# Kernel optimization log

Hardware: AMD Instinct MI355X
Metric: run time of the kernel (lower is better)

The kernel has to match this reference:

```python
import jax, jax.numpy as jnp
import numpy as np

TEMP = 0.01            # entropy temperature
THRESH = 0.92          # hamming similarity threshold
BETA = 0.25            # commitment weight
ENT_W = 0.1            # entropy loss weight


def _l2_normalize(x, axis=-1, eps=1e-12):
    n = jnp.sqrt(jnp.sum(x * x, axis=axis, keepdims=True))
    return x / jnp.maximum(n, eps)


def _entropy_loss(affinity):
    # affinity: [N, K] codebook affinities (cosine similarities)
    fa = affinity / TEMP
    probs = jax.nn.softmax(fa, axis=-1)
    log_probs = jax.nn.log_softmax(fa + 1e-5, axis=-1)
    avg_probs = jnp.mean(probs, axis=0)
    avg_entropy = -jnp.sum(avg_probs * jnp.log(avg_probs + 1e-5))
    sample_entropy = -jnp.mean(jnp.sum(probs * log_probs, axis=-1))
    return sample_entropy - avg_entropy


def _hamming_consistency_loss(input_blocks, z_e):
    # binary occupancy: non-air voxels -> 1
    binary = (jnp.argmax(input_blocks, axis=1) != 0).astype(jnp.float32)  # [B,24,24,24]
    B = binary.shape[0]
    # faithful to torch: plain reshapes (no transpose)
    patterns = binary.reshape(B, 6, 4, 6, 4, 6, 4).reshape(B, 6, 6, 6, 64).reshape(-1, 64)
    N = patterns.shape[0]
    P = patterns
    # pairwise hamming distance via two Gram matmuls
    ham = P @ (1.0 - P).T + (1.0 - P) @ P.T          # [N,N]
    sim = 1.0 - ham / 64.0
    mask = (sim > THRESH) & (~jnp.eye(N, dtype=bool))
    W = jax.lax.stop_gradient(jnp.where(mask, sim, 0.0))  # detached weights
    # pre-quant embeddings per chunk, l2-normalized; cosine distance matrix
    emb = jnp.transpose(z_e, (0, 2, 3, 4, 1)).reshape(N, -1)  # [N, C]
    en = _l2_normalize(emb, axis=1)
    cos = en @ en.T                                   # [N,N]
    dist = 1.0 - cos
    return jnp.sum(dist * W) / (jnp.sum(W) + 1e-8)


def setup_inputs() -> dict:
    key = jax.random.key(0)
    k1, k2, k3 = jax.random.split(key, 3)
    input_blocks = jax.random.normal(k1, (16, 32, 24, 24, 24), dtype=jnp.float32)
    z_e = jax.random.normal(k2, (16, 256, 6, 6, 6), dtype=jnp.float32)
    codebook = jax.random.normal(k3, (1024, 256), dtype=jnp.float32)
    return {"input_blocks": input_blocks, "z_e": z_e, "codebook": codebook}


def reference(input_blocks, z_e, codebook):
    B, C, H, W, D = z_e.shape
    z = jnp.transpose(z_e, (0, 2, 3, 4, 1)).reshape(-1, C)   # [N, C]
    zn = _l2_normalize(z, axis=1)
    en = _l2_normalize(codebook, axis=1)                      # [K, C]
    affinity = zn @ en.T                                      # [N, K]
    idx = jnp.argmax(affinity, axis=1)                        # max cosine == min L2 on sphere
    z_q = en[idx]                                             # [N, C]
    sg = jax.lax.stop_gradient
    codebook_loss = jnp.mean((z_q - sg(zn)) ** 2)
    commit_loss = BETA * jnp.mean((sg(z_q) - zn) ** 2)
    ent_loss = ENT_W * _entropy_loss(affinity)
    ham_loss = _hamming_consistency_loss(input_blocks, z_e)
    loss = codebook_loss + commit_loss + ent_loss + ham_loss
    # straight-through estimator
    z_q_ste = zn + sg(z_q - zn)
    z_q_out = jnp.transpose(z_q_ste.reshape(B, H, W, D, C), (0, 4, 1, 2, 3))
    return z_q_out, loss, idx
```

## Files before the change

### kernel.cpp

```cpp
#include <hip/hip_runtime.h>
#include <cstdint>
#include <cstddef>

#define N_ROWS 3456
#define C_DIM 256
#define K_CB 1024
#define B_SZ 16
#define SPATIAL 216
#define VOX 13824
#define NCH 32
#define N_GBLK 108
#define N_FBLK 486

typedef __attribute__((ext_vector_type(16))) float f32x16;
typedef __attribute__((ext_vector_type(8))) short bf16x8;

__device__ __forceinline__ unsigned short f2bf_rne(float f) {
    unsigned int u = __float_as_uint(f);
    u += 0x7FFFu + ((u >> 16) & 1u);
    return (unsigned short)(u >> 16);
}
__device__ __forceinline__ float bf2f(unsigned short h) {
    unsigned int u = ((unsigned int)h) << 16;
    return __uint_as_float(u);
}

__device__ __forceinline__ size_t swz(int n, int c) {
    return (size_t)(n >> 5) * 8192 + (size_t)((c >> 3) * 256) + (size_t)((n & 31) * 8) + (c & 7);
}

__global__ __launch_bounds__(256) void k_pre(
        const float* __restrict__ in, const float* __restrict__ cb,
        const float* __restrict__ ze,
        unsigned long long* __restrict__ pats,
        float* __restrict__ scal,
        float* __restrict__ en,
        unsigned short* __restrict__ ehi, unsigned short* __restrict__ elo,
        unsigned short* __restrict__ zhi, unsigned short* __restrict__ zlo) {
    int bid = blockIdx.x;
    int t = threadIdx.x;
    if (bid < 432) {
        if (bid == 0 && t < 16) scal[t] = 0.0f;
        __shared__ unsigned long long wpk[8];
        if (t < 8) wpk[t] = 0ULL;
        __syncthreads();
        int v0i = bid * 512 + t * 2;
        int b = v0i / VOX;
        int r = v0i % VOX;
        const float* p = in + (size_t)b * NCH * VOX + r;
        float2 vals[NCH];
#pragma unroll
        for (int c = 0; c < NCH; ++c)
            vals[c] = *(const float2*)&p[(size_t)c * VOX];
        float m0 = vals[1].x, m1 = vals[1].y;
#pragma unroll
        for (int c = 2; c < NCH; ++c) {
            m0 = fmaxf(m0, vals[c].x);
            m1 = fmaxf(m1, vals[c].y);
        }
        unsigned long long bits = (m0 > vals[0].x ? 1ULL : 0ULL)
                                | (m1 > vals[0].y ? 2ULL : 0ULL);
        atomicOr(&wpk[t >> 5], bits << ((t & 31) * 2));
        __syncthreads();
        if (t < 8) pats[(bid * 512 >> 6) + t] = wpk[t];
        return;
    }
    __shared__ float ws[16];
    if (bid < 1456) {
        int k = bid - 432, c = t;
        float v = cb[k * C_DIM + c];
        float ss = v * v;
#pragma unroll
        for (int off = 32; off > 0; off >>= 1) ss += __shfl_down(ss, off, 64);
        if ((c & 63) == 0) ws[c >> 6] = ss;
        __syncthreads();
        float nrm = fmaxf(sqrtf(ws[0] + ws[1] + ws[2] + ws[3]), 1e-12f);
        float o = v / nrm;
        en[k * C_DIM + c] = o;
        unsigned short h = f2bf_rne(o);
        size_t off = swz(k, c);
        ehi[off] = h;
        elo[off] = f2bf_rne(o - bf2f(h));
    } else {
        int zb = bid - 1456;
        int n0 = zb * 4;
        int b = n0 / SPATIAL, s0 = n0 - b * SPATIAL;
        int c = t, w = t >> 6, lane = t & 63;
        float4 v4 = *(const float4*)&ze[((size_t)(b * C_DIM + c)) * SPATIAL + s0];
        float q0 = v4.x * v4.x, q1 = v4.y * v4.y, q2 = v4.z * v4.z, q3 = v4.w * v4.w;
#pragma unroll
        for (int off = 32; off > 0; off >>= 1) {
            q0 += __shfl_down(q0, off, 64);
            q1 += __shfl_down(q1, off, 64);
            q2 += __shfl_down(q2, off, 64);
            q3 += __shfl_down(q3, off, 64);
        }
        if (lane == 0) {
            ws[w * 4 + 0] = q0; ws[w * 4 + 1] = q1;
            ws[w * 4 + 2] = q2; ws[w * 4 + 3] = q3;
        }
        __syncthreads();
        float vv[4] = {v4.x, v4.y, v4.z, v4.w};
#pragma unroll
        for (int j = 0; j < 4; ++j) {
            float nrm = fmaxf(sqrtf(ws[j] + ws[4 + j] + ws[8 + j] + ws[12 + j]), 1e-12f);
            float o = vv[j] / nrm;
            unsigned short h = f2bf_rne(o);
            size_t off = swz(n0 + j, c);
            zhi[off] = h;
            zlo[off] = f2bf_rne(o - bf2f(h));
        }
    }
}

__global__ __launch_bounds__(512) void k_fat(
        const unsigned short* __restrict__ zhi, const unsigned short* __restrict__ zlo,
        const unsigned short* __restrict__ ehi, const unsigned short* __restrict__ elo,
        const unsigned long long* __restrict__ pats,
        const float* __restrict__ en,
        float* __restrict__ avgp_part, float* __restrict__ scal,
        float* __restrict__ out) {
    __shared__ float zq[32 * 257];
    __shared__ float sm[32][8];
    __shared__ int   si[32][8];
    __shared__ float sS[32][8];
    __shared__ float sT[32][8];
    __shared__ float gm[32];
    __shared__ int   gmi[32];
    __shared__ float invS[32];
    __shared__ float ws8[8];
    __shared__ float hw8[8], hd8[8];
    __shared__ int lastflag;
    unsigned int* done = (unsigned int*)&scal[8];

    int t = threadIdx.x;
    int w = t >> 6, lane = t & 63;
    int half = lane >> 5, l31 = lane & 31;

    int bid0 = blockIdx.x;
    int xcd = bid0 & 7, slot = bid0 >> 3;
    int bid;
    if (bid0 < 432) {
        if (xcd < 2) bid = slot * 2 + xcd;
        else         bid = N_GBLK + slot * 6 + (xcd - 2);
    } else {
        bid = N_GBLK + 324 + (bid0 - 432);
    }

    const bf16x8* __restrict__ Zh = (const bf16x8*)zhi;
    const bf16x8* __restrict__ Zl = (const bf16x8*)zlo;
    const bf16x8* __restrict__ Eh = (const bf16x8*)ehi;
    const bf16x8* __restrict__ El = (const bf16x8*)elo;

    if (bid < N_GBLK) {
        int sa = bid;
        int n0 = bid * 32;
        int boff = (bid * 5) & 15;

        f32x16 acc[4];
#pragma unroll
        for (int q = 0; q < 4; ++q)
#pragma unroll
            for (int e = 0; e < 16; ++e) acc[q][e] = 0.0f;

#pragma unroll
        for (int s = 0; s < 16; ++s) {
            int s16 = (s + boff) & 15;
            int u = s16 * 64 + lane;
            bf16x8 ah = Zh[(size_t)sa * 1024 + u];
            bf16x8 al = Zl[(size_t)sa * 1024 + u];
            bf16x8 bh[4], bl[4];
#pragma unroll
            for (int q = 0; q < 4; ++q) {
                bh[q] = Eh[(size_t)(w * 4 + q) * 1024 + u];
                bl[q] = El[(size_t)(w * 4 + q) * 1024 + u];
            }
#pragma unroll
            for (int q = 0; q < 4; ++q) {
                acc[q] = __builtin_amdgcn_mfma_f32_32x32x16_bf16(ah, bh[q], acc[q], 0, 0, 0);
                acc[q] = __builtin_amdgcn_mfma_f32_32x32x16_bf16(ah, bl[q], acc[q], 0, 0, 0);
                acc[q] = __builtin_amdgcn_mfma_f32_32x32x16_bf16(al, bh[q], acc[q], 0, 0, 0);
            }
        }

#pragma unroll
        for (int g = 0; g < 16; ++g) {
            float m = acc[0][g];
            int mi = w * 128 + l31;
#pragma unroll
            for (int q = 1; q < 4; ++q) {
                float x = acc[q][g];
                int c = w * 128 + q * 32 + l31;
                if (x > m) { m = x; mi = c; }
            }
#pragma unroll
            for (int mask = 1; mask < 32; mask <<= 1) {
                float vo = __shfl_xor(m, mask, 64);
                int   io = __shfl_xor(mi, mask, 64);
                if (vo > m || (vo == m && io < mi)) { m = vo; mi = io; }
            }
            int row = (g & 3) + 8 * (g >> 2) + 4 * half;
            if (l31 == 0) { sm[row][w] = m; si[row][w] = mi; }
        }
        __syncthreads();

        float cmv = 0.0f;
        if (t < 32) {
            float m = sm[t][0];
            int mi = si[t][0];
#pragma unroll
            for (int ww = 1; ww < 8; ++ww) {
                float mw = sm[t][ww];
                int miw = si[t][ww];
                if (mw > m || (mw == m && miw < mi)) { m = mw; mi = miw; }
            }
            gm[t] = m; gmi[t] = mi;
            out[884737 + n0 + t] = (float)mi;
            cmv = 2.0f - 2.0f * m;
        }
        if (w == 0) {
#pragma unroll
            for (int off = 32; off > 0; off >>= 1) cmv += __shfl_down(cmv, off, 64);
            if (lane == 0) atomicAdd(&scal[1], cmv);
        }
        __syncthreads();

#pragma unroll
        for (int g = 0; g < 16; ++g) {
            int row = (g & 3) + 8 * (g >> 2) + 4 * half;
            float gmr = gm[row];
            float S = 0.0f, T = 0.0f;
#pragma unroll
            for (int q = 0; q < 4; ++q) {
                float d = 100.0f * (acc[q][g] - gmr);
                float ee = __expf(d);
                S += ee; T += ee * d;
                acc[q][g] = ee;
            }
#pragma unroll
            for (int mask = 1; mask < 32; mask <<= 1) {
                S += __shfl_xor(S, mask, 64);
                T += __shfl_xor(T, mask, 64);
            }
            if (l31 == 0) { sS[row][w] = S; sT[row][w] = T; }
        }
#pragma unroll
        for (int rr = 0; rr < 4; ++rr) {
            int row = w * 4 + rr;
            int mi = gmi[row];
            float4 g4 = *(const float4*)&en[(size_t)mi * C_DIM + lane * 4];
            zq[row * 257 + lane * 4 + 0] = g4.x;
            zq[row * 257 + lane * 4 + 1] = g4.y;
            zq[row * 257 + lane * 4 + 2] = g4.z;
            zq[row * 257 + lane * 4 + 3] = g4.w;
        }
        __syncthreads();

        float sev = 0.0f;
        if (t < 32) {
            float S = 0.0f, T = 0.0f;
#pragma unroll
            for (int ww = 0; ww < 8; ++ww) { S += sS[t][ww]; T += sT[t][ww]; }
            float iv = 1.0f / S;
            invS[t] = iv;
            sev = logf(S) - T * iv;
        }
        if (w == 0) {
#pragma unroll
            for (int off = 32; off > 0; off >>= 1) sev += __shfl_down(sev, off, 64);
            if (lane == 0) atomicAdd(&scal[0], sev);
        }
        __syncthreads();

        {
            float cs[4] = {0.0f, 0.0f, 0.0f, 0.0f};
#pragma unroll
            for (int g = 0; g < 16; ++g) {
                int row = (g & 3) + 8 * (g >> 2) + 4 * half;
                float iv = invS[row];
#pragma unroll
                for (int q = 0; q < 4; ++q) cs[q] += acc[q][g] * iv;
            }
#pragma unroll
            for (int q = 0; q < 4; ++q) cs[q] += __shfl_xor(cs[q], 32, 64);
            if (half == 0) {
#pragma unroll
                for (int q = 0; q < 4; ++q)
                    avgp_part[(size_t)bid * K_CB + w * 128 + q * 32 + l31] = cs[q];
            }
        }

        {
            int rl = t & 31, cg = t >> 5;
            int n = n0 + rl;
            int b = n / SPATIAL, s = n - b * SPATIAL;
            size_t obase = ((size_t)b * C_DIM) * SPATIAL + s;
#pragma unroll
            for (int cc = 0; cc < 16; ++cc) {
                int c = cg * 16 + cc;
                out[obase + (size_t)c * SPATIAL] = zq[rl * 257 + c];
            }
        }
    } else {
        int hb = bid - N_GBLK;
        int ti = 0, rem = hb;
        while (rem >= 27 - ti) { rem -= 27 - ti; ++ti; }
        int tj = ti + rem;
        int i0 = ti * 128, j0 = tj * 128;
        float factor = (ti == tj) ? 1.0f : 2.0f;
        int iw = w & 3, kh = w >> 2;
        int sib = ti * 4 + iw;
        int sjb = tj * 4;
        int hoff = hb & 7;

        f32x16 acc[4];
#pragma unroll
        for (int c = 0; c < 4; ++c)
#pragma unroll
            for (int e = 0; e < 16; ++e) acc[c][e] = 0.0f;

#pragma unroll
        for (int s8 = 0; s8 < 8; ++s8) {
            int u = (kh * 8 + ((s8 + hoff) & 7)) * 64 + lane;
            bf16x8 a0 = Zh[(size_t)sib * 1024 + u];
            bf16x8 bf[4];
#pragma unroll
            for (int c = 0; c < 4; ++c)
                bf[c] = Zh[(size_t)(sjb + c) * 1024 + u];
#pragma unroll
            for (int c = 0; c < 4; ++c)
                acc[c] = __builtin_amdgcn_mfma_f32_32x32x16_bf16(a0, bf[c], acc[c], 0, 0, 0);
        }

        unsigned long long pj[4];
#pragma unroll
        for (int c = 0; c < 4; ++c) pj[c] = pats[j0 + c * 32 + l31];

        float sW = 0.0f, sD = 0.0f;
        int ibase = i0 + iw * 32 + 4 * half;
#pragma unroll
        for (int g = 0; g < 16; ++g) {
            int gi = ibase + (g & 3) + 8 * (g >> 2);
            unsigned long long pi = pats[gi];
#pragma unroll
            for (int c = 0; c < 4; ++c) {
                int gj = j0 + c * 32 + l31;
                int pop = __popcll(pi ^ pj[c]);
                float wgt = (pop <= 5 && gi != gj) ? (1.0f - (float)pop * 0.015625f) : 0.0f;
                sW += wgt;
                sD += wgt * acc[c][g];
            }
        }
#pragma unroll
        for (int off = 32; off > 0; off >>= 1) {
            sW += __shfl_down(sW, off, 64);
            sD += __shfl_down(sD, off, 64);
        }
        if (lane == 0) { hw8[w] = sW; hd8[w] = sD; }
        __syncthreads();
        if (t == 0) {
            float W = hw8[0] + hw8[1] + hw8[2] + hw8[3];
            float D = hd8[0] + hd8[1] + hd8[2] + hd8[3]
                    + hd8[4] + hd8[5] + hd8[6] + hd8[7];
            atomicAdd(&scal[2], factor * W);
            atomicAdd(&scal[3], factor * D);
        }
    }

    __syncthreads();
    if (t == 0) {
        __threadfence();
        unsigned int old = atomicAdd(done, 1u);
        lastflag = (old == N_FBLK - 1) ? 1 : 0;
    }
    __syncthreads();
    if (lastflag) {
        __threadfence();
        int col0 = t, col1 = t + 512;
        float p0 = 0.0f, p1 = 0.0f, p2 = 0.0f, p3 = 0.0f;
        float q0 = 0.0f, q1 = 0.0f, q2 = 0.0f, q3 = 0.0f;
        for (int bb = 0; bb < N_GBLK; bb += 4) {
            p0 += avgp_part[(size_t)(bb + 0) * K_CB + col0];
            p1 += avgp_part[(size_t)(bb + 1) * K_CB + col0];
            p2 += avgp_part[(size_t)(bb + 2) * K_CB + col0];
            p3 += avgp_part[(size_t)(bb + 3) * K_CB + col0];
            q0 += avgp_part[(size_t)(bb + 0) * K_CB + col1];
            q1 += avgp_part[(size_t)(bb + 1) * K_CB + col1];
            q2 += avgp_part[(size_t)(bb + 2) * K_CB + col1];
            q3 += avgp_part[(size_t)(bb + 3) * K_CB + col1];
        }
        float ap0 = (p0 + p1 + p2 + p3) * (1.0f / N_ROWS);
        float ap1 = (q0 + q1 + q2 + q3) * (1.0f / N_ROWS);
        float term = ap0 * logf(ap0 + 1e-5f) + ap1 * logf(ap1 + 1e-5f);
#pragma unroll
        for (int off = 32; off > 0; off >>= 1) term += __shfl_down(term, off, 64);
        if (lane == 0) ws8[w] = term;
        __syncthreads();
        if (t == 0) {
            float sAP = 0.0f;
#pragma unroll
            for (int i = 0; i < 8; ++i) sAP += ws8[i];
            float s0 = atomicAdd(&scal[0], 0.0f);
            float s1 = atomicAdd(&scal[1], 0.0f);
            float s2 = atomicAdd(&scal[2], 0.0f);
            float s3 = atomicAdd(&scal[3], 0.0f);
            float sample = s0 * (1.0f / N_ROWS);
            float commit = s1 * (1.0f / ((float)N_ROWS * C_DIM));
            float ent = 0.1f * (sample + sAP);
            float ham = (s2 - s3) / (s2 + 1e-8f);
            out[884736] = 1.25f * commit + ent + ham;
        }
    }
}

extern "C" void kernel_launch(void* const* d_in, const int* in_sizes, int n_in,
                              void* d_out, int out_size, void* d_ws, size_t ws_size,
                              hipStream_t stream) {
    const float* in_blocks = (const float*)d_in[0];
    const float* z_e       = (const float*)d_in[1];
    const float* cb        = (const float*)d_in[2];
    float* out = (float*)d_out;

    char* ws = (char*)d_ws;
    float* en   = (float*)(ws + 0);
    unsigned short* zhi = (unsigned short*)(ws + 15204352);
    unsigned short* zlo = (unsigned short*)(ws + 16973824);
    unsigned short* ehi = (unsigned short*)(ws + 18743296);
    unsigned short* elo = (unsigned short*)(ws + 19267584);
    unsigned long long* pats = (unsigned long long*)(ws + 19791872);
    float* avgp_part = (float*)(ws + 19819520);
    float* scal = (float*)(ws + 20704256);

    k_pre<<<2320, 256, 0, stream>>>(in_blocks, cb, z_e, pats, scal,
                                    en, ehi, elo, zhi, zlo);
    k_fat<<<N_FBLK, 512, 0, stream>>>(zhi, zlo, ehi, elo, pats, en,
                                      avgp_part, scal, out);
}
```

Measured before the change: 153.8 us.

## Double block size to 1024 threads with split-K across wave halves

Launches the fused kernel with 1024 threads per block. In the codebook-affinity path the K dimension is split between two halves of the waves, and the halves' partial accumulators are merged through a 64KB shared buffer in two parity passes. In the Hamming Gram path K is split four ways instead of two. The XCD-aware block remapping and staggered K offsets are removed. The intent is to shorten each block's serial MFMA chain and raise parallelism per block. The cost is extra shared-memory traffic, more barriers, and higher LDS and register pressure that may lower occupancy.

```diff
diff --git a/kernel.cpp b/kernel.cpp
--- a/kernel.cpp
+++ b/kernel.cpp
@@ -113,14 +113,14 @@
     }
 }
 
-__global__ __launch_bounds__(512) void k_fat(
+__global__ __launch_bounds__(1024) void k_fat(
         const unsigned short* __restrict__ zhi, const unsigned short* __restrict__ zlo,
         const unsigned short* __restrict__ ehi, const unsigned short* __restrict__ elo,
         const unsigned long long* __restrict__ pats,
         const float* __restrict__ en,
         float* __restrict__ avgp_part, float* __restrict__ scal,
         float* __restrict__ out) {
-    __shared__ float zq[32 * 257];
+    __shared__ float mrg[16384];
     __shared__ float sm[32][8];
     __shared__ int   si[32][8];
     __shared__ float sS[32][8];
@@ -128,25 +128,16 @@
     __shared__ float gm[32];
     __shared__ int   gmi[32];
     __shared__ float invS[32];
-    __shared__ float ws8[8];
-    __shared__ float hw8[8], hd8[8];
+    __shared__ float ws16[16];
+    __shared__ float hw16[16], hd16[16];
     __shared__ int lastflag;
     unsigned int* done = (unsigned int*)&scal[8];
+    float* zq = mrg;
 
     int t = threadIdx.x;
     int w = t >> 6, lane = t & 63;
     int half = lane >> 5, l31 = lane & 31;
-
-    int bid0 = blockIdx.x;
-    int xcd = bid0 & 7, slot = bid0 >> 3;
-    int bid;
-    if (bid0 < 432) {
-        if (xcd < 2) bid = slot * 2 + xcd;
-        else         bid = N_GBLK + slot * 6 + (xcd - 2);
-    } else {
-        bid = N_GBLK + 324 + (bid0 - 432);
-    }
-
+    int bid = blockIdx.x;
     const bf16x8* __restrict__ Zh = (const bf16x8*)zhi;
     const bf16x8* __restrict__ Zl = (const bf16x8*)zlo;
     const bf16x8* __restrict__ Eh = (const bf16x8*)ehi;
@@ -155,7 +146,7 @@
     if (bid < N_GBLK) {
         int sa = bid;
         int n0 = bid * 32;
-        int boff = (bid * 5) & 15;
+        int cg = w & 7, kh = w >> 3;
 
         f32x16 acc[4];
 #pragma unroll
@@ -164,16 +155,15 @@
             for (int e = 0; e < 16; ++e) acc[q][e] = 0.0f;
 
 #pragma unroll
-        for (int s = 0; s < 16; ++s) {
-            int s16 = (s + boff) & 15;
-            int u = s16 * 64 + lane;
+        for (int s = 0; s < 8; ++s) {
+            int u = (kh * 8 + s) * 64 + lane;
             bf16x8 ah = Zh[(size_t)sa * 1024 + u];
             bf16x8 al = Zl[(size_t)sa * 1024 + u];
             bf16x8 bh[4], bl[4];
 #pragma unroll
             for (int q = 0; q < 4; ++q) {
-                bh[q] = Eh[(size_t)(w * 4 + q) * 1024 + u];
-                bl[q] = El[(size_t)(w * 4 + q) * 1024 + u];
+                bh[q] = Eh[(size_t)(cg * 4 + q) * 1024 + u];
+                bl[q] = El[(size_t)(cg * 4 + q) * 1024 + u];
             }
 #pragma unroll
             for (int q = 0; q < 4; ++q) {
@@ -184,23 +174,47 @@
         }
 
 #pragma unroll
-        for (int g = 0; g < 16; ++g) {
-            float m = acc[0][g];
-            int mi = w * 128 + l31;
-#pragma unroll
-            for (int q = 1; q < 4; ++q) {
-                float x = acc[q][g];
-                int c = w * 128 + q * 32 + l31;
-                if (x > m) { m = x; mi = c; }
-            }
-#pragma unroll
-            for (int mask = 1; mask < 32; mask <<= 1) {
-                float vo = __shfl_xor(m, mask, 64);
-                int   io = __shfl_xor(mi, mask, 64);
-                if (vo > m || (vo == m && io < mi)) { m = vo; mi = io; }
-            }
-            int row = (g & 3) + 8 * (g >> 2) + 4 * half;
-            if (l31 == 0) { sm[row][w] = m; si[row][w] = mi; }
+        for (int par = 0; par < 2; ++par) {
+            if (kh == 1 && (cg & 1) == par) {
+                int slot = cg >> 1;
+#pragma unroll
+                for (int q = 0; q < 4; ++q)
+#pragma unroll
+                    for (int g = 0; g < 16; ++g)
+                        mrg[slot * 4096 + (q * 16 + g) * 64 + lane] = acc[q][g];
+            }
+            __syncthreads();
+            if (kh == 0 && (cg & 1) == par) {
+                int slot = cg >> 1;
+#pragma unroll
+                for (int q = 0; q < 4; ++q)
+#pragma unroll
+                    for (int g = 0; g < 16; ++g)
+                        acc[q][g] += mrg[slot * 4096 + (q * 16 + g) * 64 + lane];
+            }
+            __syncthreads();
+        }
+
+        if (w < 8) {
+#pragma unroll
+            for (int g = 0; g < 16; ++g) {
+                float m = acc[0][g];
+                int mi = cg * 128 + l31;
+#pragma unroll
+                for (int q = 1; q < 4; ++q) {
+                    float x = acc[q][g];
+                    int c = cg * 128 + q * 32 + l31;
+                    if (x > m) { m = x; mi = c; }
+                }
+#pragma unroll
+                for (int mask = 1; mask < 32; mask <<= 1) {
+                    float vo = __shfl_xor(m, mask, 64);
+                    int   io = __shfl_xor(mi, mask, 64);
+                    if (vo > m || (vo == m && io < mi)) { m = vo; mi = io; }
+                }
+                int row = (g & 3) + 8 * (g >> 2) + 4 * half;
+                if (l31 == 0) { sm[row][cg] = m; si[row][cg] = mi; }
+            }
         }
         __syncthreads();
 
@@ -225,34 +239,36 @@
         }
         __syncthreads();
 
-#pragma unroll
-        for (int g = 0; g < 16; ++g) {
-            int row = (g & 3) + 8 * (g >> 2) + 4 * half;
-            float gmr = gm[row];
-            float S = 0.0f, T = 0.0f;
-#pragma unroll
-            for (int q = 0; q < 4; ++q) {
-                float d = 100.0f * (acc[q][g] - gmr);
-                float ee = __expf(d);
-                S += ee; T += ee * d;
-                acc[q][g] = ee;
-            }
-#pragma unroll
-            for (int mask = 1; mask < 32; mask <<= 1) {
-                S += __shfl_xor(S, mask, 64);
-                T += __shfl_xor(T, mask, 64);
-            }
-            if (l31 == 0) { sS[row][w] = S; sT[row][w] = T; }
-        }
-#pragma unroll
-        for (int rr = 0; rr < 4; ++rr) {
-            int row = w * 4 + rr;
-            int mi = gmi[row];
-            float4 g4 = *(const float4*)&en[(size_t)mi * C_DIM + lane * 4];
-            zq[row * 257 + lane * 4 + 0] = g4.x;
-            zq[row * 257 + lane * 4 + 1] = g4.y;
-            zq[row * 257 + lane * 4 + 2] = g4.z;
-            zq[row * 257 + lane * 4 + 3] = g4.w;
+        if (w < 8) {
+#pragma unroll
+            for (int g = 0; g < 16; ++g) {
+                int row = (g & 3) + 8 * (g >> 2) + 4 * half;
+                float gmr = gm[row];
+                float S = 0.0f, T = 0.0f;
+#pragma unroll
+                for (int q = 0; q < 4; ++q) {
+                    float d = 100.0f * (acc[q][g] - gmr);
+                    float ee = __expf(d);
+                    S += ee; T += ee * d;
+                    acc[q][g] = ee;
+                }
+#pragma unroll
+                for (int mask = 1; mask < 32; mask <<= 1) {
+                    S += __shfl_xor(S, mask, 64);
+                    T += __shfl_xor(T, mask, 64);
+                }
+                if (l31 == 0) { sS[row][cg] = S; sT[row][cg] = T; }
+            }
+#pragma unroll
+            for (int rr = 0; rr < 4; ++rr) {
+                int row = cg * 4 + rr;
+                int mi = gmi[row];
+                float4 g4 = *(const float4*)&en[(size_t)mi * C_DIM + lane * 4];
+                zq[row * 257 + lane * 4 + 0] = g4.x;
+                zq[row * 257 + lane * 4 + 1] = g4.y;
+                zq[row * 257 + lane * 4 + 2] = g4.z;
+                zq[row * 257 + lane * 4 + 3] = g4.w;
+            }
         }
         __syncthreads();
 
@@ -272,7 +288,7 @@
         }
         __syncthreads();
 
-        {
+        if (w < 8) {
             float cs[4] = {0.0f, 0.0f, 0.0f, 0.0f};
 #pragma unroll
             for (int g = 0; g < 16; ++g) {
@@ -286,18 +302,18 @@
             if (half == 0) {
 #pragma unroll
                 for (int q = 0; q < 4; ++q)
-                    avgp_part[(size_t)bid * K_CB + w * 128 + q * 32 + l31] = cs[q];
+                    avgp_part[(size_t)bid * K_CB + cg * 128 + q * 32 + l31] = cs[q];
             }
         }
 
         {
-            int rl = t & 31, cg = t >> 5;
+            int rl = t & 31, cg32 = t >> 5;
             int n = n0 + rl;
             int b = n / SPATIAL, s = n - b * SPATIAL;
             size_t obase = ((size_t)b * C_DIM) * SPATIAL + s;
 #pragma unroll
-            for (int cc = 0; cc < 16; ++cc) {
-                int c = cg * 16 + cc;
+            for (int cc = 0; cc < 8; ++cc) {
+                int c = cg32 * 8 + cc;
                 out[obase + (size_t)c * SPATIAL] = zq[rl * 257 + c];
             }
         }
@@ -308,10 +324,9 @@
         int tj = ti + rem;
         int i0 = ti * 128, j0 = tj * 128;
         float factor = (ti == tj) ? 1.0f : 2.0f;
-        int iw = w & 3, kh = w >> 2;
+        int iw = w & 3, kq = w >> 2;
         int sib = ti * 4 + iw;
         int sjb = tj * 4;
-        int hoff = hb & 7;
 
         f32x16 acc[4];
 #pragma unroll
@@ -320,8 +335,8 @@
             for (int e = 0; e < 16; ++e) acc[c][e] = 0.0f;
 
 #pragma unroll
-        for (int s8 = 0; s8 < 8; ++s8) {
-            int u = (kh * 8 + ((s8 + hoff) & 7)) * 64 + lane;
+        for (int s4 = 0; s4 < 4; ++s4) {
+            int u = (kq * 4 + s4) * 64 + lane;
             bf16x8 a0 = Zh[(size_t)sib * 1024 + u];
             bf16x8 bf[4];
 #pragma unroll
@@ -356,12 +371,13 @@
             sW += __shfl_down(sW, off, 64);
             sD += __shfl_down(sD, off, 64);
         }
-        if (lane == 0) { hw8[w] = sW; hd8[w] = sD; }
+        if (lane == 0) { hw16[w] = sW; hd16[w] = sD; }
         __syncthreads();
         if (t == 0) {
-            float W = hw8[0] + hw8[1] + hw8[2] + hw8[3];
-            float D = hd8[0] + hd8[1] + hd8[2] + hd8[3]
-                    + hd8[4] + hd8[5] + hd8[6] + hd8[7];
+            float W = hw16[0] + hw16[1] + hw16[2] + hw16[3];
+            float D = 0.0f;
+#pragma unroll
+            for (int i = 0; i < 16; ++i) D += hd16[i];
             atomicAdd(&scal[2], factor * W);
             atomicAdd(&scal[3], factor * D);
         }
@@ -376,30 +392,24 @@
     __syncthreads();
     if (lastflag) {
         __threadfence();
-        int col0 = t, col1 = t + 512;
+        int col = t;
         float p0 = 0.0f, p1 = 0.0f, p2 = 0.0f, p3 = 0.0f;
-        float q0 = 0.0f, q1 = 0.0f, q2 = 0.0f, q3 = 0.0f;
         for (int bb = 0; bb < N_GBLK; bb += 4) {
-            p0 += avgp_part[(size_t)(bb + 0) * K_CB + col0];
-            p1 += avgp_part[(size_t)(bb + 1) * K_CB + col0];
-            p2 += avgp_part[(size_t)(bb + 2) * K_CB + col0];
-            p3 += avgp_part[(size_t)(bb + 3) * K_CB + col0];
-            q0 += avgp_part[(size_t)(bb + 0) * K_CB + col1];
-            q1 += avgp_part[(size_t)(bb + 1) * K_CB + col1];
-            q2 += avgp_part[(size_t)(bb + 2) * K_CB + col1];
-            q3 += avgp_part[(size_t)(bb + 3) * K_CB + col1];
-        }
-        float ap0 = (p0 + p1 + p2 + p3) * (1.0f / N_ROWS);
-        float ap1 = (q0 + q1 + q2 + q3) * (1.0f / N_ROWS);
-        float term = ap0 * logf(ap0 + 1e-5f) + ap1 * logf(ap1 + 1e-5f);
+            p0 += avgp_part[(size_t)(bb + 0) * K_CB + col];
+            p1 += avgp_part[(size_t)(bb + 1) * K_CB + col];
+            p2 += avgp_part[(size_t)(bb + 2) * K_CB + col];
+            p3 += avgp_part[(size_t)(bb + 3) * K_CB + col];
+        }
+        float ap = (p0 + p1 + p2 + p3) * (1.0f / N_ROWS);
+        float term = ap * logf(ap + 1e-5f);
 #pragma unroll
         for (int off = 32; off > 0; off >>= 1) term += __shfl_down(term, off, 64);
-        if (lane == 0) ws8[w] = term;
+        if (lane == 0) ws16[w] = term;
         __syncthreads();
         if (t == 0) {
             float sAP = 0.0f;
 #pragma unroll
-            for (int i = 0; i < 8; ++i) sAP += ws8[i];
+            for (int i = 0; i < 16; ++i) sAP += ws16[i];
             float s0 = atomicAdd(&scal[0], 0.0f);
             float s1 = atomicAdd(&scal[1], 0.0f);
             float s2 = atomicAdd(&scal[2], 0.0f);
@@ -433,6 +443,6 @@
 
     k_pre<<<2320, 256, 0, stream>>>(in_blocks, cb, z_e, pats, scal,
                                     en, ehi, elo, zhi, zlo);
-    k_fat<<<N_FBLK, 512, 0, stream>>>(zhi, zlo, ehi, elo, pats, en,
-                                      avgp_part, scal, out);
-}
+    k_fat<<<N_FBLK, 1024, 0, stream>>>(zhi, zlo, ehi, elo, pats, en,
+                                       avgp_part, scal, out);
+}
```

Result: faster. 136.5 us (-11.3%).
